# Kernel tuning notes

Measured on AMD Instinct MI355X. Metric: run time of the kernel, lower is better.

Reference implementation:

```python
import jax, jax.numpy as jnp
import numpy as np
from jax import lax

EPS = 1e-5

def _instance_norm(x):
    # per-sample, per-channel over HW, affine=False (torch default), biased var
    m = jnp.mean(x, axis=(2, 3), keepdims=True)
    v = jnp.mean((x - m) ** 2, axis=(2, 3), keepdims=True)
    return (x - m) / jnp.sqrt(v + EPS)

def _lrelu(x):
    return jax.nn.leaky_relu(x, 0.2)

def _conv(x, w, b, stride=1, pad=0):
    y = lax.conv_general_dilated(x, w, (stride, stride), ((pad, pad), (pad, pad)),
                                 dimension_numbers=('NCHW', 'OIHW', 'NCHW'))
    return y + b[None, :, None, None]

def _conv_transpose(x, w, b):
    # torch ConvTranspose2d(k=3, stride=2, padding=1, output_padding=1)
    # == dilated conv with lhs_dilation=2, pad (k-1-p, k-1-p+op) = (1, 2),
    # kernel spatially flipped and in/out swapped. w: (Cin, Cout, 3, 3)
    wt = jnp.flip(w, axis=(2, 3)).transpose(1, 0, 2, 3)  # (Cout, Cin, 3, 3)
    y = lax.conv_general_dilated(x, wt, (1, 1), ((1, 2), (1, 2)),
                                 lhs_dilation=(2, 2),
                                 dimension_numbers=('NCHW', 'OIHW', 'NCHW'))
    return y + b[None, :, None, None]

def _reflect_pad1(x):
    return jnp.pad(x, ((0, 0), (0, 0), (1, 1), (1, 1)), mode='reflect')

def _nearest_resize(x, out_h, out_w):
    in_h, in_w = x.shape[2], x.shape[3]
    iy = (jnp.arange(out_h) * (in_h / out_h)).astype(jnp.int32)
    ix = (jnp.arange(out_w) * (in_w / out_w)).astype(jnp.int32)
    return x[:, :, iy][:, :, :, ix]

def setup_inputs() -> dict:
    key = jax.random.key(0)
    ks = jax.random.split(key, 12)
    B, S, H, W = 8, 19, 256, 256
    out_nc = 512
    inp = jax.random.normal(ks[0], (B, 3, H, W), dtype=jnp.float32)
    labels = jax.random.randint(ks[1], (B, 1, H, W), 0, S)
    segmap = (labels == jnp.arange(S).reshape(1, S, 1, 1)).astype(jnp.float32)
    sc = 0.05
    return {
        'input': inp, 'segmap': segmap,
        'w1': jax.random.normal(ks[2], (32, 3, 3, 3), jnp.float32) * sc,
        'b1': jnp.zeros((32,), jnp.float32),
        'w2': jax.random.normal(ks[3], (64, 32, 3, 3), jnp.float32) * sc,
        'b2': jnp.zeros((64,), jnp.float32),
        'w3': jax.random.normal(ks[4], (128, 64, 3, 3), jnp.float32) * sc,
        'b3': jnp.zeros((128,), jnp.float32),
        'w4': jax.random.normal(ks[5], (128, 256, 3, 3), jnp.float32) * sc,  # torch convT layout (Cin, Cout, kh, kw)
        'b4': jnp.zeros((256,), jnp.float32),
        'w5': jax.random.normal(ks[6], (out_nc, 256, 3, 3), jnp.float32) * sc,
        'b5': jnp.zeros((out_nc,), jnp.float32),
    }

def _backbone(x, w1, b1, w2, b2, w3, b3, w4, b4, w5, b5):
    x = _lrelu(_instance_norm(_conv(_reflect_pad1(x), w1, b1)))          # [B,32,256,256]
    x = _lrelu(_instance_norm(_conv(x, w2, b2, stride=2, pad=1)))        # [B,64,128,128]
    x = _lrelu(_instance_norm(_conv(x, w3, b3, stride=2, pad=1)))        # [B,128,64,64]
    x = _lrelu(_instance_norm(_conv_transpose(x, w4, b4)))               # [B,256,128,128]
    x = jnp.tanh(_conv(_reflect_pad1(x), w5, b5))                        # [B,512,128,128]
    return x

def reference(input, segmap, w1, b1, w2, b2, w3, b3, w4, b4, w5, b5):
    codes = _backbone(input, w1, b1, w2, b2, w3, b3, w4, b4, w5, b5)
    seg = _nearest_resize(segmap, codes.shape[2], codes.shape[3])
    mask = (seg > 0).astype(codes.dtype)                                  # segmap.bool()
    sums = jnp.einsum('bchw,bshw->bsc', codes, mask)                      # masked sum per (b, class)
    counts = jnp.sum(mask, axis=(2, 3))[:, :, None]                       # [B,S,1]
    return jnp.where(counts > 0, sums / jnp.maximum(counts, 1.0), 0.0)    # [B,S,C]
```

## Files before the change

### kernel.cpp

```cpp
#include <hip/hip_runtime.h>

#define LB __launch_bounds__(256)

constexpr int S = 19;

typedef __attribute__((ext_vector_type(8))) short frag16;
typedef __attribute__((ext_vector_type(8))) ushort ushort8;
typedef __attribute__((ext_vector_type(4))) float f32x4;

__device__ __forceinline__ int reflect256(int i) { return i < 0 ? -i : (i > 255 ? 510 - i : i); }
__device__ __forceinline__ int reflect128(int i) { return i < 0 ? -i : (i > 127 ? 254 - i : i); }

__device__ __forceinline__ ushort f2bf(float f) {
    union { float f; uint u; } a; a.f = f;
    uint r = a.u + 0x7fffu + ((a.u >> 16) & 1u);
    return (ushort)(r >> 16);
}
__device__ __forceinline__ float bf2f(ushort u) {
    union { uint u; float f; } a; a.u = ((uint)u) << 16; return a.f;
}

__device__ __forceinline__ void gll16(const void* g, void* l) {
    __builtin_amdgcn_global_load_lds(
        (const __attribute__((address_space(1))) void*)g,
        (__attribute__((address_space(3))) void*)l, 16, 0, 0);
}

__global__ LB void k_conv1cl(const float* __restrict__ in, const float* __restrict__ w,
                             const float* __restrict__ bias, ushort* __restrict__ out) {
    __shared__ float Wr[864];
    __shared__ float Bs[32];
    int t = threadIdx.x;
    for (int e = t; e < 864; e += 256) Wr[e] = w[e];
    if (t < 32) Bs[t] = bias[t];
    __syncthreads();
    int idx = blockIdx.x * 256 + t;
    int x = idx & 255, y = (idx >> 8) & 255, b = idx >> 16;
    float v[27];
    #pragma unroll
    for (int ci = 0; ci < 3; ++ci) {
        const float* ip = in + ((b * 3 + ci) << 16);
        #pragma unroll
        for (int ky = 0; ky < 3; ++ky) {
            int iy = reflect256(y + ky - 1);
            #pragma unroll
            for (int kx = 0; kx < 3; ++kx) {
                int ix = reflect256(x + kx - 1);
                v[ci * 9 + ky * 3 + kx] = ip[(iy << 8) + ix];
            }
        }
    }
    ushort* op = out + (long)idx * 32;
    #pragma unroll
    for (int g = 0; g < 4; ++g) {
        ushort8 o;
        #pragma unroll
        for (int j = 0; j < 8; ++j) {
            int co = g * 8 + j;
            float a = Bs[co];
            #pragma unroll
            for (int k = 0; k < 27; ++k) a += v[k] * Wr[co * 27 + k];
            o[j] = f2bf(a);
        }
        *(ushort8*)(op + g * 8) = o;
    }
}

template <int C, int PB, int SPLITS>
__global__ LB void k_stats_cl(const ushort* __restrict__ x,
                              float* __restrict__ psum, float* __restrict__ pss) {
    __shared__ float lsum[C], lss[C];
    int b = blockIdx.x / SPLITS, sp = blockIdx.x % SPLITS;
    int t = threadIdx.x;
    if (t < C) { lsum[t] = 0.f; lss[t] = 0.f; }
    __syncthreads();
    constexpr int CG = C / 8;
    constexpr int PO = 256 / CG;
    int c0 = (t % CG) * 8;
    int po = t / CG;
    float s[8], ss[8];
    #pragma unroll
    for (int k = 0; k < 8; ++k) { s[k] = 0.f; ss[k] = 0.f; }
    const ushort* base = x + ((long)b * SPLITS + sp) * (long)PB * C;
    for (int p = po; p < PB; p += PO) {
        ushort8 v = *(const ushort8*)(base + (long)p * C + c0);
        #pragma unroll
        for (int k = 0; k < 8; ++k) {
            float f = bf2f(v[k]);
            s[k] += f; ss[k] += f * f;
        }
    }
    #pragma unroll
    for (int k = 0; k < 8; ++k) {
        atomicAdd(&lsum[c0 + k], s[k]);
        atomicAdd(&lss[c0 + k], ss[k]);
    }
    __syncthreads();
    if (t < C) {
        psum[blockIdx.x * C + t] = lsum[t];
        pss[blockIdx.x * C + t] = lss[t];
    }
}

template <int C, int SPLITS, int P>
__global__ LB void k_red_cl(const float* __restrict__ psum, const float* __restrict__ pss,
                            float* __restrict__ mean, float* __restrict__ istd) {
    int idx = blockIdx.x * 256 + threadIdx.x;
    if (idx >= 8 * C) return;
    int b = idx / C, c = idx % C;
    float s = 0.f, ss = 0.f;
    for (int sp = 0; sp < SPLITS; ++sp) {
        s += psum[(b * SPLITS + sp) * C + c];
        ss += pss[(b * SPLITS + sp) * C + c];
    }
    float m = s / (float)P;
    float v = ss / (float)P - m * m;
    mean[idx] = m;
    istd[idx] = rsqrtf(v + 1e-5f);
}

template <int C, int P>
__global__ LB void k_nl_cl(ushort* __restrict__ x, const float* __restrict__ mean,
                           const float* __restrict__ istd) {
    long e = ((long)blockIdx.x * 256 + threadIdx.x) * 8;
    int c0 = (int)(e % C);
    int b = (int)(e / ((long)P * C));
    ushort8 v = *(ushort8*)(x + e);
    const float* mp = mean + b * C + c0;
    const float* ip = istd + b * C + c0;
    #pragma unroll
    for (int k = 0; k < 8; ++k) {
        float u = (bf2f(v[k]) - mp[k]) * ip[k];
        u = u > 0.f ? u : 0.2f * u;
        v[k] = f2bf(u);
    }
    *(ushort8*)(x + e) = v;
}

__global__ LB void k_wtall(const float* __restrict__ w2, const float* __restrict__ w3,
                           const float* __restrict__ w4, const float* __restrict__ w5,
                           ushort* __restrict__ t2, ushort* __restrict__ t3,
                           ushort* __restrict__ t4, ushort* __restrict__ t5) {
    int e = blockIdx.x * 256 + threadIdx.x;
    if (e < 18432) {
        int ci = e & 31, co = (e >> 5) & 63, tap = e >> 11;
        t2[e] = f2bf(w2[(co * 32 + ci) * 9 + tap]);
    } else if (e < 18432 + 73728) {
        int e2 = e - 18432;
        int ci = e2 & 63, co = (e2 >> 6) & 127, tap = e2 >> 13;
        t3[e2] = f2bf(w3[(co * 64 + ci) * 9 + tap]);
    } else if (e < 18432 + 73728 + 294912) {
        int e3 = e - (18432 + 73728);
        int ci = e3 & 127, co = (e3 >> 7) & 255, tap = e3 >> 15;
        t4[e3] = f2bf(w4[ci * 2304 + co * 9 + tap]);
    } else {
        int e4 = e - (18432 + 73728 + 294912);
        int ci = e4 & 255, co = (e4 >> 8) & 511, tap = e4 >> 17;
        t5[e4] = f2bf(w5[(co * 256 + ci) * 9 + tap]);
    }
}

__global__ LB void k_conv2m(const ushort* __restrict__ xin, const ushort* __restrict__ wt,
                            const float* __restrict__ bias, ushort* __restrict__ xout) {
    int bx = blockIdx.x;
    int y = bx & 127, b = bx >> 7;
    int t = threadIdx.x, w = t >> 6, lane = t & 63;
    int col0 = w * 32;
    int lanep = lane & 15, hi = lane >> 4;

    f32x4 acc[4][2];
    #pragma unroll
    for (int m = 0; m < 4; ++m)
        #pragma unroll
        for (int n = 0; n < 2; ++n) acc[m][n] = (f32x4){0.f, 0.f, 0.f, 0.f};

    #pragma unroll
    for (int ky = 0; ky < 3; ++ky) {
        int iy = 2 * y + ky - 1;
        if (iy < 0) continue;
        #pragma unroll
        for (int kx = 0; kx < 3; ++kx) {
            int tap = ky * 3 + kx;
            const ushort* wb = wt + ((tap * 64 + lanep) << 5) + hi * 8;
            frag16 av[4];
            #pragma unroll
            for (int m = 0; m < 4; ++m) av[m] = *(const frag16*)(wb + ((m * 16) << 5));
            frag16 bv[2];
            #pragma unroll
            for (int n = 0; n < 2; ++n) {
                int xo = col0 + n * 16 + lanep;
                int ix = 2 * xo + kx - 1;
                frag16 vv = (frag16)(short)0;
                if (ix >= 0)
                    vv = *(const frag16*)(xin + ((((long)(b * 256 + iy)) << 8) + ix) * 32 + hi * 8);
                bv[n] = vv;
            }
            #pragma unroll
            for (int m = 0; m < 4; ++m)
                #pragma unroll
                for (int n = 0; n < 2; ++n)
                    acc[m][n] = __builtin_amdgcn_mfma_f32_16x16x32_bf16(av[m], bv[n], acc[m][n], 0, 0, 0);
        }
    }
    float bvv[4][4];
    #pragma unroll
    for (int m = 0; m < 4; ++m)
        #pragma unroll
        for (int r = 0; r < 4; ++r) bvv[m][r] = bias[m * 16 + hi * 4 + r];
    #pragma unroll
    for (int n = 0; n < 2; ++n) {
        int xo = col0 + n * 16 + lanep;
        long pb = ((((long)(b * 128 + y)) << 7) + xo) * 64 + hi * 4;
        #pragma unroll
        for (int m = 0; m < 4; ++m) {
            ushort4 o;
            o.x = f2bf(acc[m][n][0] + bvv[m][0]);
            o.y = f2bf(acc[m][n][1] + bvv[m][1]);
            o.z = f2bf(acc[m][n][2] + bvv[m][2]);
            o.w = f2bf(acc[m][n][3] + bvv[m][3]);
            *(ushort4*)(xout + pb + m * 16) = o;
        }
    }
}

__global__ LB void k_conv3m(const ushort* __restrict__ xin, const ushort* __restrict__ wt,
                            const float* __restrict__ bias, ushort* __restrict__ xout) {
    int bx = blockIdx.x;
    int y = bx & 63, b = bx >> 6;
    int t = threadIdx.x, w = t >> 6, lane = t & 63;
    int co0 = (w >> 1) * 64;
    int col0 = (w & 1) * 32;
    int lanep = lane & 15, hi = lane >> 4;

    f32x4 acc[4][2];
    #pragma unroll
    for (int m = 0; m < 4; ++m)
        #pragma unroll
        for (int n = 0; n < 2; ++n) acc[m][n] = (f32x4){0.f, 0.f, 0.f, 0.f};

    #pragma unroll
    for (int ky = 0; ky < 3; ++ky) {
        int iy = 2 * y + ky - 1;
        if (iy < 0) continue;
        #pragma unroll
        for (int kx = 0; kx < 3; ++kx) {
            int tap = ky * 3 + kx;
            #pragma unroll
            for (int ck = 0; ck < 2; ++ck) {
                int ci0 = ck * 32;
                const ushort* wb = wt + ((tap * 128 + co0 + lanep) << 6) + ci0 + hi * 8;
                frag16 av[4];
                #pragma unroll
                for (int m = 0; m < 4; ++m) av[m] = *(const frag16*)(wb + ((m * 16) << 6));
                frag16 bv[2];
                #pragma unroll
                for (int n = 0; n < 2; ++n) {
                    int xo = col0 + n * 16 + lanep;
                    int ix = 2 * xo + kx - 1;
                    frag16 vv = (frag16)(short)0;
                    if (ix >= 0)
                        vv = *(const frag16*)(xin + ((((long)(b * 128 + iy)) << 7) + ix) * 64 + ci0 + hi * 8);
                    bv[n] = vv;
                }
                #pragma unroll
                for (int m = 0; m < 4; ++m)
                    #pragma unroll
                    for (int n = 0; n < 2; ++n)
                        acc[m][n] = __builtin_amdgcn_mfma_f32_16x16x32_bf16(av[m], bv[n], acc[m][n], 0, 0, 0);
            }
        }
    }
    float bvv[4][4];
    #pragma unroll
    for (int m = 0; m < 4; ++m)
        #pragma unroll
        for (int r = 0; r < 4; ++r) bvv[m][r] = bias[co0 + m * 16 + hi * 4 + r];
    #pragma unroll
    for (int n = 0; n < 2; ++n) {
        int xo = col0 + n * 16 + lanep;
        long pb = ((((long)(b * 64 + y)) << 6) + xo) * 128 + co0 + hi * 4;
        #pragma unroll
        for (int m = 0; m < 4; ++m) {
            ushort4 o;
            o.x = f2bf(acc[m][n][0] + bvv[m][0]);
            o.y = f2bf(acc[m][n][1] + bvv[m][1]);
            o.z = f2bf(acc[m][n][2] + bvv[m][2]);
            o.w = f2bf(acc[m][n][3] + bvv[m][3]);
            *(ushort4*)(xout + pb + m * 16) = o;
        }
    }
}

__global__ LB void k_convt4m(const ushort* __restrict__ x3l, const ushort* __restrict__ wt,
                             const float* __restrict__ bias, ushort* __restrict__ xl) {
    int bx = blockIdx.x;
    int parity = bx & 3;
    int py = parity >> 1, px = parity & 1;
    int rg = (bx >> 2) & 15;
    int ct = (bx >> 6) & 3;
    int b  = bx >> 8;
    int co0 = ct * 64;
    int t = threadIdx.x;
    int w = t >> 6;
    int ip = rg * 4 + w;
    int lane = t & 63;
    int lanep = lane & 15;
    int hi = lane >> 4;
    int laneq = hi * 8;

    f32x4 acc[4][4];
    #pragma unroll
    for (int m = 0; m < 4; ++m)
        #pragma unroll
        for (int n = 0; n < 4; ++n) acc[m][n] = (f32x4){0.f, 0.f, 0.f, 0.f};

    #pragma unroll
    for (int ky = 0; ky < 3; ++ky) {
        if (((ky + py) & 1) == 0) continue;
        int i = ip + ((py == 1 && ky == 0) ? 1 : 0);
        if (i >= 64) continue;
        #pragma unroll
        for (int kx = 0; kx < 3; ++kx) {
            if (((kx + px) & 1) == 0) continue;
            int dxp = (px == 1 && kx == 0) ? 1 : 0;
            int tap = ky * 3 + kx;
            const ushort* wbase = wt + (((long)tap * 256 + co0 + lanep) << 7) + laneq;
            const ushort* xbase = x3l + ((((long)b << 12) + (i << 6)) << 7) + laneq;
            #pragma unroll
            for (int ci0 = 0; ci0 < 128; ci0 += 32) {
                frag16 av[4], bv[4];
                #pragma unroll
                for (int m = 0; m < 4; ++m)
                    av[m] = *(const frag16*)(wbase + ((m * 16) << 7) + ci0);
                #pragma unroll
                for (int n = 0; n < 4; ++n) {
                    int j = n * 16 + lanep + dxp;
                    bool valid = j < 64;
                    frag16 v = *(const frag16*)(xbase + ((valid ? j : 63) << 7) + ci0);
                    if (!valid) v = (frag16)(short)0;
                    bv[n] = v;
                }
                #pragma unroll
                for (int m = 0; m < 4; ++m)
                    #pragma unroll
                    for (int n = 0; n < 4; ++n)
                        acc[m][n] = __builtin_amdgcn_mfma_f32_16x16x32_bf16(av[m], bv[n], acc[m][n], 0, 0, 0);
            }
        }
    }

    float bvv[4][4];
    #pragma unroll
    for (int m = 0; m < 4; ++m)
        #pragma unroll
        for (int r = 0; r < 4; ++r)
            bvv[m][r] = bias[co0 + m * 16 + hi * 4 + r];
    int y = 2 * ip + py;
    #pragma unroll
    for (int n = 0; n < 4; ++n) {
        int x = 2 * (n * 16 + lanep) + px;
        long pb = ((((long)b << 14) + (y << 7) + x) << 8) + co0 + hi * 4;
        #pragma unroll
        for (int m = 0; m < 4; ++m) {
            ushort4 o;
            o.x = f2bf(acc[m][n][0] + bvv[m][0]);
            o.y = f2bf(acc[m][n][1] + bvv[m][1]);
            o.z = f2bf(acc[m][n][2] + bvv[m][2]);
            o.w = f2bf(acc[m][n][3] + bvv[m][3]);
            *(ushort4*)(xl + pb + m * 16) = o;
        }
    }
}

__global__ LB void k_label(const float* __restrict__ segmap, int* __restrict__ lab,
                           int* __restrict__ counts) {
    __shared__ int h[S];
    if (threadIdx.x < S) h[threadIdx.x] = 0;
    __syncthreads();
    int idx = blockIdx.x * 256 + threadIdx.x;
    int x = idx & 127, y = (idx >> 7) & 127, b = idx >> 14;
    const float* sp = segmap + (long)b * S * 65536 + (y << 1) * 256 + (x << 1);
    int s = 0;
    for (int c = 0; c < S; ++c) {
        if (sp[c * 65536] > 0.f) { s = c; break; }
    }
    lab[idx] = s;
    atomicAdd(&h[s], 1);
    __syncthreads();
    if (threadIdx.x < S) atomicAdd(&counts[b * S + threadIdx.x], h[threadIdx.x]);
}

__global__ void __launch_bounds__(256, 2)
k_conv5m(const ushort* __restrict__ xl, const ushort* __restrict__ wt,
         const float* __restrict__ bias, const int* __restrict__ lab,
         float* __restrict__ sumbuf) {
    __shared__ __align__(16) ushort L[35072];
    float* part = (float*)L;
    constexpr int XS = 0, WS = 16640;

    int bx = blockIdx.x;
    int yp = bx & 63;
    int ct = (bx >> 6) & 7;
    int b  = bx >> 9;
    int y0 = yp * 2, cob = ct * 64;
    int t = threadIdx.x;
    int w = t >> 6;
    int lane = t & 63;
    int row_w = w & 1;
    int col0 = (w >> 1) * 64;
    int lanep = lane & 15;
    int hi = lane >> 4;
    int xw8 = (hi ^ ((lanep >> 1) & 3)) * 8;

    long xbase = (long)b << 14;
    long xg[9]; int wg[9];
    #pragma unroll
    for (int k = 0; k < 9; ++k) {
        int e = t + k * 256;
        int q = e & 3, p = e >> 2;
        int qp = q ^ ((p >> 1) & 3);
        if (e < 2080) {
            int r = p / 130, c = p - r * 130;
            int gy = reflect128(y0 - 1 + r);
            int gc = reflect128(c - 1);
            xg[k] = ((xbase + (gy << 7) + gc) << 8) + qp * 8;
        } else xg[k] = xbase << 8;
        wg[k] = (((p >> 6) * 512 + cob + (p & 63)) << 8) + qp * 8;
    }

    f32x4 acc[4][4];
    #pragma unroll
    for (int m = 0; m < 4; ++m)
        #pragma unroll
        for (int n = 0; n < 4; ++n) acc[m][n] = (f32x4){0.f, 0.f, 0.f, 0.f};

    #pragma unroll 1
    for (int c8 = 0; c8 < 8; ++c8) {
        int cin = c8 * 32;
        #pragma unroll
        for (int k = 0; k < 8; ++k) gll16(xl + xg[k] + cin, L + XS + ((k << 8) + t) * 8);
        if (t < 32) gll16(xl + xg[8] + cin, L + XS + ((8 << 8) + t) * 8);
        #pragma unroll
        for (int k = 0; k < 9; ++k) gll16(wt + wg[k] + cin, L + WS + ((k << 8) + t) * 8);
        __syncthreads();
        #pragma unroll
        for (int tap = 0; tap < 9; ++tap) {
            int ky = tap / 3, kx = tap % 3;
            frag16 av[4];
            #pragma unroll
            for (int m = 0; m < 4; ++m)
                av[m] = *(const frag16*)(L + WS + (tap * 64 + m * 16 + lanep) * 32 + xw8);
            int p0 = (row_w + ky) * 130 + col0 + kx + lanep;
            int bo = p0 * 32 + (hi ^ ((p0 >> 1) & 3)) * 8;
            frag16 bf[4];
            #pragma unroll
            for (int n = 0; n < 4; ++n)
                bf[n] = *(const frag16*)(L + XS + bo + n * 512);
            #pragma unroll
            for (int m = 0; m < 4; ++m)
                #pragma unroll
                for (int n = 0; n < 4; ++n)
                    acc[m][n] = __builtin_amdgcn_mfma_f32_16x16x32_bf16(av[m], bf[n], acc[m][n], 0, 0, 0);
        }
        __syncthreads();
    }

    float bv[4][4];
    #pragma unroll
    for (int m = 0; m < 4; ++m)
        #pragma unroll
        for (int r = 0; r < 4; ++r)
            bv[m][r] = bias[cob + m * 16 + hi * 4 + r];

    for (int e = t; e < S * 64; e += 256) part[e] = 0.f;
    __syncthreads();

    int y = y0 + row_w;
    #pragma unroll
    for (int n = 0; n < 4; ++n) {
        int x = col0 + n * 16 + lanep;
        int s = lab[(b << 14) + (y << 7) + x];
        #pragma unroll
        for (int m = 0; m < 4; ++m)
            #pragma unroll
            for (int r = 0; r < 4; ++r)
                atomicAdd(&part[s * 64 + m * 16 + hi * 4 + r], tanhf(acc[m][n][r] + bv[m][r]));
    }
    __syncthreads();
    for (int e = t; e < S * 64; e += 256) {
        int s = e >> 6, col = e & 63;
        atomicAdd(&sumbuf[((b * S + s) << 9) + cob + col], part[e]);
    }
}

__global__ LB void k_final(const float* __restrict__ sumbuf, const int* __restrict__ counts,
                           float* __restrict__ out) {
    int idx = blockIdx.x * 256 + threadIdx.x;
    int tt = idx >> 9;
    int s = tt % S, b = tt / S;
    int cnt = counts[b * S + s];
    out[idx] = cnt > 0 ? sumbuf[idx] / (float)cnt : 0.f;
}

extern "C" void kernel_launch(void* const* d_in, const int* in_sizes, int n_in,
                              void* d_out, int out_size, void* d_ws, size_t ws_size,
                              hipStream_t stream) {
    const float* input  = (const float*)d_in[0];
    const float* segmap = (const float*)d_in[1];
    const float* w1 = (const float*)d_in[2];  const float* b1 = (const float*)d_in[3];
    const float* w2 = (const float*)d_in[4];  const float* b2 = (const float*)d_in[5];
    const float* w3 = (const float*)d_in[6];  const float* b3 = (const float*)d_in[7];
    const float* w4 = (const float*)d_in[8];  const float* b4 = (const float*)d_in[9];
    const float* w5 = (const float*)d_in[10]; const float* b5 = (const float*)d_in[11];
    float* out = (float*)d_out;

    float* ws = (float*)d_ws;
    ushort* xl    = (ushort*)ws;
    ushort* x1l   = (ushort*)(ws + 16777216);
    ushort* x2l   = (ushort*)(ws + 25165824);
    ushort* x3l   = (ushort*)(ws + 29360128);
    float* sumbuf = ws + 31457280;
    float* mean   = ws + 31535104;
    float* istd   = ws + 31537152;
    int*   lab    = (int*)(ws + 31539200);
    int*   counts = (int*)(ws + 31670272);
    ushort* wt5   = (ushort*)(ws + 31670528);
    ushort* wt4t  = (ushort*)(ws + 32260352);
    ushort* wt2   = (ushort*)(ws + 32407808);
    ushort* wt3   = (ushort*)(ws + 32417024);
    float* psum   = ws + 32453888;
    float* pss    = ws + 32519424;

    hipMemsetAsync(sumbuf, 0, 77824 * sizeof(float), stream);
    hipMemsetAsync(counts, 0, 256 * sizeof(int), stream);

    k_wtall<<<6120, 256, 0, stream>>>(w2, w3, w4, w5, wt2, wt3, wt4t, wt5);
    k_conv1cl<<<2048, 256, 0, stream>>>(input, w1, b1, x1l);
    k_stats_cl<32, 1024, 64><<<512, 256, 0, stream>>>(x1l, psum, pss);
    k_red_cl<32, 64, 65536><<<1, 256, 0, stream>>>(psum, pss, mean, istd);
    k_nl_cl<32, 65536><<<8192, 256, 0, stream>>>(x1l, mean, istd);
    k_conv2m<<<1024, 256, 0, stream>>>(x1l, wt2, b2, x2l);
    k_stats_cl<64, 512, 32><<<256, 256, 0, stream>>>(x2l, psum, pss);
    k_red_cl<64, 32, 16384><<<2, 256, 0, stream>>>(psum, pss, mean, istd);
    k_nl_cl<64, 16384><<<4096, 256, 0, stream>>>(x2l, mean, istd);
    k_conv3m<<<512, 256, 0, stream>>>(x2l, wt3, b3, x3l);
    k_stats_cl<128, 256, 16><<<128, 256, 0, stream>>>(x3l, psum, pss);
    k_red_cl<128, 16, 4096><<<4, 256, 0, stream>>>(psum, pss, mean, istd);
    k_nl_cl<128, 4096><<<2048, 256, 0, stream>>>(x3l, mean, istd);
    k_convt4m<<<2048, 256, 0, stream>>>(x3l, wt4t, b4, xl);
    k_stats_cl<256, 512, 32><<<256, 256, 0, stream>>>(xl, psum, pss);
    k_red_cl<256, 32, 16384><<<8, 256, 0, stream>>>(psum, pss, mean, istd);
    k_nl_cl<256, 16384><<<16384, 256, 0, stream>>>(xl, mean, istd);
    k_label<<<512, 256, 0, stream>>>(segmap, lab, counts);
    k_conv5m<<<4096, 256, 0, stream>>>(xl, wt5, b5, lab, sumbuf);
    k_final<<<304, 256, 0, stream>>>(sumbuf, counts, out);
}
```

Baseline: 908.0 us.

## Double-buffer conv5 LDS loads and widen tile to 128 output channels

The final conv+tanh+masked-sum kernel now uses 512-thread blocks that each cover 128 output channels instead of 64, so every input tile loaded into LDS is reused by twice as many channels. Input and weight tiles are double-buffered in LDS, with weights streamed per kernel row, so the next global-to-LDS loads overlap with the MFMA work on the current buffer. Synchronisation is done by hand with explicit vmcnt waits and scheduling barriers. In exchange, LDS use rises to about 113KB, allowing only one block per CU, and correctness now depends on the hand-counted wait values.

```diff
diff --git a/kernel.cpp b/kernel.cpp
--- a/kernel.cpp
+++ b/kernel.cpp
@@ -390,42 +390,59 @@
     if (threadIdx.x < S) atomicAdd(&counts[b * S + threadIdx.x], h[threadIdx.x]);
 }
 
-__global__ void __launch_bounds__(256, 2)
+__global__ void __launch_bounds__(512, 1)
 k_conv5m(const ushort* __restrict__ xl, const ushort* __restrict__ wt,
          const float* __restrict__ bias, const int* __restrict__ lab,
          float* __restrict__ sumbuf) {
-    __shared__ __align__(16) ushort L[35072];
+    __shared__ __align__(16) ushort L[57856];
     float* part = (float*)L;
-    constexpr int XS = 0, WS = 16640;
+    constexpr int XS0 = 0, XS1 = 16640, WS0 = 33280, WS1 = 45568;
 
     int bx = blockIdx.x;
     int yp = bx & 63;
-    int ct = (bx >> 6) & 7;
-    int b  = bx >> 9;
-    int y0 = yp * 2, cob = ct * 64;
+    int ct = (bx >> 6) & 3;
+    int b  = bx >> 8;
+    int y0 = yp * 2, cob = ct * 128;
     int t = threadIdx.x;
     int w = t >> 6;
     int lane = t & 63;
     int row_w = w & 1;
-    int col0 = (w >> 1) * 64;
+    int col0 = ((w >> 1) & 1) * 64;
+    int coh = w >> 2;
+    int cobw = cob + coh * 64;
     int lanep = lane & 15;
     int hi = lane >> 4;
-    int xw8 = (hi ^ ((lanep >> 1) & 3)) * 8;
+    int wkey8 = (hi ^ ((lanep >> 1) & 3)) * 8;
 
     long xbase = (long)b << 14;
-    long xg[9]; int wg[9];
-    #pragma unroll
-    for (int k = 0; k < 9; ++k) {
-        int e = t + k * 256;
+    long xg[4]; long xgt = 0;
+    #pragma unroll
+    for (int k = 0; k < 4; ++k) {
+        int e = t + k * 512;
         int q = e & 3, p = e >> 2;
         int qp = q ^ ((p >> 1) & 3);
-        if (e < 2080) {
-            int r = p / 130, c = p - r * 130;
-            int gy = reflect128(y0 - 1 + r);
-            int gc = reflect128(c - 1);
-            xg[k] = ((xbase + (gy << 7) + gc) << 8) + qp * 8;
-        } else xg[k] = xbase << 8;
-        wg[k] = (((p >> 6) * 512 + cob + (p & 63)) << 8) + qp * 8;
+        int r = p / 130, c = p - r * 130;
+        int gy = reflect128(y0 - 1 + r);
+        int gc = reflect128(c - 1);
+        xg[k] = ((xbase + (gy << 7) + gc) << 8) + qp * 8;
+    }
+    if (t < 32) {
+        int e = 2048 + t;
+        int q = e & 3, p = e >> 2;
+        int qp = q ^ ((p >> 1) & 3);
+        int r = p / 130, c = p - r * 130;
+        int gy = reflect128(y0 - 1 + r);
+        int gc = reflect128(c - 1);
+        xgt = ((xbase + (gy << 7) + gc) << 8) + qp * 8;
+    }
+    int wgb[3];
+    #pragma unroll
+    for (int k = 0; k < 3; ++k) {
+        int f = t + k * 512;
+        int q = f & 3, p = f >> 2;
+        int qp = q ^ ((p >> 1) & 3);
+        int tapin = p >> 7, co = p & 127;
+        wgb[k] = ((tapin * 512 + cob + co) << 8) + qp * 8;
     }
 
     f32x4 acc[4][4];
@@ -434,48 +451,91 @@
         #pragma unroll
         for (int n = 0; n < 4; ++n) acc[m][n] = (f32x4){0.f, 0.f, 0.f, 0.f};
 
+    #define ISSUE_X(c) {                                                              \
+        int cin = (c) * 32; int xd = ((c) & 1) ? XS1 : XS0;                           \
+        _Pragma("unroll")                                                             \
+        for (int k = 0; k < 4; ++k) gll16(xl + xg[k] + cin, L + xd + (t + k * 512) * 8); \
+        if (t < 32) gll16(xl + xgt + cin, L + xd + (2048 + t) * 8); }
+
+    #define ISSUE_W(c, g) {                                                           \
+        int cin = (c) * 32; int wd = ((3 * (c) + (g)) & 1) ? WS1 : WS0;               \
+        _Pragma("unroll")                                                             \
+        for (int k = 0; k < 3; ++k)                                                   \
+            gll16(wt + wgb[k] + (g) * 393216 + cin, L + wd + (t + k * 512) * 8); }
+
+    #define SYNC_PRE() { __builtin_amdgcn_sched_barrier(0);                           \
+        __builtin_amdgcn_s_barrier(); __builtin_amdgcn_sched_barrier(0); }
+    #define SYNC_POST() { __builtin_amdgcn_sched_barrier(0); __builtin_amdgcn_s_barrier(); }
+
+    #define COMPUTE(c, g) {                                                           \
+        const ushort* xs  = L + (((c) & 1) ? XS1 : XS0);                              \
+        const ushort* wsb = L + (((3 * (c) + (g)) & 1) ? WS1 : WS0);                  \
+        _Pragma("unroll")                                                             \
+        for (int tapin = 0; tapin < 3; ++tapin) {                                     \
+            frag16 av[4];                                                             \
+            _Pragma("unroll")                                                         \
+            for (int m = 0; m < 4; ++m)                                               \
+                av[m] = *(const frag16*)(wsb + tapin * 4096 + coh * 2048 + m * 512    \
+                                         + lanep * 32 + wkey8);                       \
+            int p0 = (row_w + (g)) * 130 + col0 + tapin + lanep;                      \
+            int bo = p0 * 32 + (hi ^ ((p0 >> 1) & 3)) * 8;                            \
+            frag16 bf[4];                                                             \
+            _Pragma("unroll")                                                         \
+            for (int n = 0; n < 4; ++n) bf[n] = *(const frag16*)(xs + bo + n * 512);  \
+            _Pragma("unroll")                                                         \
+            for (int m = 0; m < 4; ++m)                                               \
+                _Pragma("unroll")                                                     \
+                for (int n = 0; n < 4; ++n)                                           \
+                    acc[m][n] = __builtin_amdgcn_mfma_f32_16x16x32_bf16(av[m], bf[n], acc[m][n], 0, 0, 0); \
+        } }
+
+    ISSUE_X(0);
+    ISSUE_W(0, 0);
+    asm volatile("s_waitcnt vmcnt(0)" ::: "memory");
+    SYNC_PRE();
+
     #pragma unroll 1
-    for (int c8 = 0; c8 < 8; ++c8) {
-        int cin = c8 * 32;
-        #pragma unroll
-        for (int k = 0; k < 8; ++k) gll16(xl + xg[k] + cin, L + XS + ((k << 8) + t) * 8);
-        if (t < 32) gll16(xl + xg[8] + cin, L + XS + ((8 << 8) + t) * 8);
-        #pragma unroll
-        for (int k = 0; k < 9; ++k) gll16(wt + wg[k] + cin, L + WS + ((k << 8) + t) * 8);
-        __syncthreads();
-        #pragma unroll
-        for (int tap = 0; tap < 9; ++tap) {
-            int ky = tap / 3, kx = tap % 3;
-            frag16 av[4];
-            #pragma unroll
-            for (int m = 0; m < 4; ++m)
-                av[m] = *(const frag16*)(L + WS + (tap * 64 + m * 16 + lanep) * 32 + xw8);
-            int p0 = (row_w + ky) * 130 + col0 + kx + lanep;
-            int bo = p0 * 32 + (hi ^ ((p0 >> 1) & 3)) * 8;
-            frag16 bf[4];
-            #pragma unroll
-            for (int n = 0; n < 4; ++n)
-                bf[n] = *(const frag16*)(L + XS + bo + n * 512);
-            #pragma unroll
-            for (int m = 0; m < 4; ++m)
-                #pragma unroll
-                for (int n = 0; n < 4; ++n)
-                    acc[m][n] = __builtin_amdgcn_mfma_f32_16x16x32_bf16(av[m], bf[n], acc[m][n], 0, 0, 0);
-        }
-        __syncthreads();
-    }
+    for (int c = 0; c < 8; ++c) {
+        if (c < 7) { ISSUE_X(c + 1); }
+        ISSUE_W(c, 1);
+        if (c < 7) { asm volatile("s_waitcnt vmcnt(7)" ::: "memory"); }
+        else       { asm volatile("s_waitcnt vmcnt(3)" ::: "memory"); }
+        SYNC_PRE();
+        COMPUTE(c, 0);
+        SYNC_POST();
+        ISSUE_W(c, 2);
+        asm volatile("s_waitcnt vmcnt(3)" ::: "memory");
+        SYNC_PRE();
+        COMPUTE(c, 1);
+        SYNC_POST();
+        if (c < 7) {
+            ISSUE_W(c + 1, 0);
+            asm volatile("s_waitcnt vmcnt(3)" ::: "memory");
+        } else {
+            asm volatile("s_waitcnt vmcnt(0)" ::: "memory");
+        }
+        SYNC_PRE();
+        COMPUTE(c, 2);
+        SYNC_POST();
+    }
+    #undef ISSUE_X
+    #undef ISSUE_W
+    #undef COMPUTE
+    #undef SYNC_PRE
+    #undef SYNC_POST
 
     float bv[4][4];
     #pragma unroll
     for (int m = 0; m < 4; ++m)
         #pragma unroll
         for (int r = 0; r < 4; ++r)
-            bv[m][r] = bias[cob + m * 16 + hi * 4 + r];
-
-    for (int e = t; e < S * 64; e += 256) part[e] = 0.f;
+            bv[m][r] = bias[cobw + m * 16 + hi * 4 + r];
+
+    for (int e = t; e < S * 128; e += 512) part[e] = 0.f;
     __syncthreads();
 
     int y = y0 + row_w;
+    int colc = coh * 64;
     #pragma unroll
     for (int n = 0; n < 4; ++n) {
         int x = col0 + n * 16 + lanep;
@@ -484,12 +544,12 @@
         for (int m = 0; m < 4; ++m)
             #pragma unroll
             for (int r = 0; r < 4; ++r)
-                atomicAdd(&part[s * 64 + m * 16 + hi * 4 + r], tanhf(acc[m][n][r] + bv[m][r]));
+                atomicAdd(&part[s * 128 + colc + m * 16 + hi * 4 + r], tanhf(acc[m][n][r] + bv[m][r]));
     }
     __syncthreads();
-    for (int e = t; e < S * 64; e += 256) {
-        int s = e >> 6, col = e & 63;
-        atomicAdd(&sumbuf[((b * S + s) << 9) + cob + col], part[e]);
+    for (int e = t; e < S * 128; e += 512) {
+        int s = e >> 7, cc = e & 127;
+        atomicAdd(&sumbuf[((b * S + s) << 9) + cob + cc], part[e]);
     }
 }
 
@@ -552,6 +612,6 @@
     k_red_cl<256, 32, 16384><<<8, 256, 0, stream>>>(psum, pss, mean, istd);
     k_nl_cl<256, 16384><<<16384, 256, 0, stream>>>(xl, mean, istd);
     k_label<<<512, 256, 0, stream>>>(segmap, lab, counts);
-    k_conv5m<<<4096, 256, 0, stream>>>(xl, wt5, b5, lab, sumbuf);
+    k_conv5m<<<2048, 512, 0, stream>>>(xl, wt5, b5, lab, sumbuf);
     k_final<<<304, 256, 0, stream>>>(sumbuf, counts, out);
 }
```

After: 938.0 us. 1.03x slower.
